# Kernel tuning notes

Measured on AMD Instinct MI355X. Metric: run time of the kernel, lower is better.

## Reference

```python
import jax, jax.numpy as jnp
import numpy as np

N = 8192          # number of nodes
F_IN = 256        # in_features
F_OUT = 128       # out_features


def setup_inputs() -> dict:
    key = jax.random.key(0)
    k1, k2, k3, k4 = jax.random.split(key, 4)
    input = jax.random.normal(k1, (N, F_IN), dtype=jnp.float32)
    adj = jax.random.uniform(k2, (N, N), dtype=jnp.float32)
    stdv = 1.0 / np.sqrt(F_OUT)
    weight = jax.random.uniform(k3, (F_IN, F_OUT), dtype=jnp.float32, minval=-stdv, maxval=stdv)
    bias = jax.random.uniform(k4, (F_OUT,), dtype=jnp.float32, minval=-stdv, maxval=stdv)
    return {"input": input, "adj": adj, "weight": weight, "bias": bias}


def reference(input, adj, weight, bias):
    # support = X @ W  [N, F_OUT]
    support = jnp.matmul(input, weight)
    # Subgraph block decomposition over a node partition is exactly A @ support:
    # block (k,i) computes adj[S_k][:, S_i] @ support[S_i] scatter-added into rows S_k.
    output = jnp.matmul(adj, support)  # [N, F_OUT]
    return output + bias
```

## Files before the change

### kernel.cpp

```cpp
#include <hip/hip_runtime.h>
#include <hip/hip_bf16.h>

#define N_NODES 8192
#define F_IN 256
#define F_OUT 128

#define SPLITK 4
#define KQ (N_NODES / SPLITK)
#define BK 64
#define NT (KQ / BK)
#define ABYTES 16384
#define BBYTES 16384
#define BUFB (ABYTES + BBYTES)

typedef __attribute__((ext_vector_type(4))) float f32x4;
typedef __attribute__((ext_vector_type(8))) short bf16x8;
typedef __attribute__((ext_vector_type(4))) unsigned int u32x4;

static __device__ __forceinline__ short bfr(float x) {
    __hip_bfloat16 h = __float2bfloat16(x);
    union { __hip_bfloat16 h; short s; } u; u.h = h;
    return u.s;
}

static __device__ __forceinline__ void gload16(const void* g, void* l) {
    __builtin_amdgcn_global_load_lds(
        (const __attribute__((address_space(1))) unsigned int*)g,
        (__attribute__((address_space(3))) unsigned int*)l, 16, 0, 0);
}

__global__ __launch_bounds__(256) void support_kernel(
        const float* __restrict__ X, const float* __restrict__ W,
        unsigned short* __restrict__ supT) {
    __shared__ float Xs[32][68];
    __shared__ float Ws[64][128];
    const int t = threadIdx.x;
    const int n0 = blockIdx.x * 32;
    const int tc = t & 31;
    const int tr = t >> 5;
    float acc[4][4];
    #pragma unroll
    for (int i = 0; i < 4; ++i)
        #pragma unroll
        for (int j = 0; j < 4; ++j) acc[i][j] = 0.f;

    for (int k0 = 0; k0 < F_IN; k0 += 64) {
        __syncthreads();
        {
            const int r = t >> 3, kc = (t & 7) * 8;
            const float* src = X + (size_t)(n0 + r) * F_IN + k0 + kc;
            f32x4 v0 = *(const f32x4*)src;
            f32x4 v1 = *(const f32x4*)(src + 4);
            *(f32x4*)&Xs[r][kc]     = v0;
            *(f32x4*)&Xs[r][kc + 4] = v1;
        }
        {
            const int col = t & 127, kb = t >> 7;
            #pragma unroll
            for (int i = 0; i < 32; ++i) {
                const int k = kb + i * 2;
                Ws[k][col] = W[(size_t)(k0 + k) * F_OUT + col];
            }
        }
        __syncthreads();
        #pragma unroll 8
        for (int k = 0; k < 64; ++k) {
            const f32x4 b = *(const f32x4*)&Ws[k][tc * 4];
            float a[4];
            #pragma unroll
            for (int i = 0; i < 4; ++i) a[i] = Xs[tr * 4 + i][k];
            #pragma unroll
            for (int i = 0; i < 4; ++i) {
                acc[i][0] += a[i] * b.x; acc[i][1] += a[i] * b.y;
                acc[i][2] += a[i] * b.z; acc[i][3] += a[i] * b.w;
            }
        }
    }
    #pragma unroll
    for (int j = 0; j < 4; ++j) {
        const int col = tc * 4 + j;
        #pragma unroll
        for (int i = 0; i < 4; ++i) {
            supT[(size_t)col * N_NODES + n0 + tr * 4 + i] =
                (unsigned short)bfr(acc[i][j]);
        }
    }
}

__global__ __launch_bounds__(512, 4) void gcn_kernel(
        const float* __restrict__ adj, const unsigned short* __restrict__ supT,
        const float* __restrict__ bias, float* __restrict__ out) {
    __shared__ char lds[2 * BUFB];
    const int t = threadIdx.x;
    const int l = t & 63;
    const int w = t >> 6;
    const int rb = blockIdx.x & 127;
    const int h = blockIdx.x >> 7;
    const int n0 = rb * 64;
    const int k0 = h * KQ;

    const int rA0 = 8 * w + (l >> 4);
    const int rA1 = rA0 + 4;
    const char* gA0 = (const char*)adj
        + ((size_t)(n0 + rA0) * N_NODES + k0) * 4 + (((l & 15) ^ (rA0 & 15)) * 16);
    const char* gA1 = (const char*)adj
        + ((size_t)(n0 + rA1) * N_NODES + k0) * 4 + (((l & 15) ^ (rA1 & 15)) * 16);
    const char* gB0 = (const char*)supT
        + ((size_t)(16 * w + (l >> 3)) * N_NODES + k0) * 2 + (((l & 7) ^ (l >> 3)) * 16);
    const char* gB1 = gB0 + (size_t)8 * N_NODES * 2;

    const int a_d0 = w * 2048;
    const int a_d1 = a_d0 + 1024;
    const int b_d0 = ABYTES + w * 2048;
    const int b_d1 = b_d0 + 1024;

    const int wm = w >> 2, wn = w & 3;
    const int aoff0 = (wm * 32 + (l & 15)) * 256;
    const int aoff1 = aoff0 + 16 * 256;
    const int akey = l & 15;
    const int ac0 = (l >> 4) * 2;
    const int boff0 = ABYTES + (wn * 32 + (l & 15)) * 128;
    const int boff1 = boff0 + 16 * 128;
    const int bkey = l & 7;
    const int cb0 = l >> 4;

    f32x4 acc00 = {0.f,0.f,0.f,0.f}, acc01 = {0.f,0.f,0.f,0.f};
    f32x4 acc10 = {0.f,0.f,0.f,0.f}, acc11 = {0.f,0.f,0.f,0.f};

#define PK(dst, a, b) \
    asm("v_cvt_pk_bf16_f32 %0, %1, %2" : "=v"(dst) : "v"(a), "v"(b))

#define STAGE(BUF) { \
    char* bb = &lds[(BUF) * BUFB]; \
    gload16(gA0, bb + a_d0); \
    gload16(gA1, bb + a_d1); \
    gload16(gB0, bb + b_d0); \
    gload16(gB1, bb + b_d1); \
    gA0 += 256; gA1 += 256; gB0 += 128; gB1 += 128; }

#define FENCE_BARRIER() { \
    asm volatile("s_waitcnt vmcnt(0)" ::: "memory"); \
    __builtin_amdgcn_sched_barrier(0); \
    __builtin_amdgcn_s_barrier(); \
    __builtin_amdgcn_sched_barrier(0); }

    STAGE(0);
    FENCE_BARRIER();

    for (int tt = 0; tt < NT; ++tt) {
        if (tt + 1 < NT) STAGE((tt + 1) & 1);

        const char* buf = &lds[(tt & 1) * BUFB];
        #pragma unroll
        for (int ks = 0; ks < 2; ++ks) {
            const int ca = ks * 8 + ac0;
            f32x4 a0lo = *(const f32x4*)(buf + aoff0 + (((ca    ) ^ akey) * 16));
            f32x4 a0hi = *(const f32x4*)(buf + aoff0 + (((ca + 1) ^ akey) * 16));
            f32x4 a1lo = *(const f32x4*)(buf + aoff1 + (((ca    ) ^ akey) * 16));
            f32x4 a1hi = *(const f32x4*)(buf + aoff1 + (((ca + 1) ^ akey) * 16));
            const int cb = ks * 4 + cb0;
            bf16x8 b0 = *(const bf16x8*)(buf + boff0 + ((cb ^ bkey) * 16));
            bf16x8 b1 = *(const bf16x8*)(buf + boff1 + ((cb ^ bkey) * 16));
            u32x4 p0, p1;
            PK(p0.x, a0lo.x, a0lo.y); PK(p0.y, a0lo.z, a0lo.w);
            PK(p0.z, a0hi.x, a0hi.y); PK(p0.w, a0hi.z, a0hi.w);
            PK(p1.x, a1lo.x, a1lo.y); PK(p1.y, a1lo.z, a1lo.w);
            PK(p1.z, a1hi.x, a1hi.y); PK(p1.w, a1hi.z, a1hi.w);
            bf16x8 am0 = __builtin_bit_cast(bf16x8, p0);
            bf16x8 am1 = __builtin_bit_cast(bf16x8, p1);
            acc00 = __builtin_amdgcn_mfma_f32_16x16x32_bf16(am0, b0, acc00, 0, 0, 0);
            acc01 = __builtin_amdgcn_mfma_f32_16x16x32_bf16(am0, b1, acc01, 0, 0, 0);
            acc10 = __builtin_amdgcn_mfma_f32_16x16x32_bf16(am1, b0, acc10, 0, 0, 0);
            acc11 = __builtin_amdgcn_mfma_f32_16x16x32_bf16(am1, b1, acc11, 0, 0, 0);
        }
        FENCE_BARRIER();
    }
#undef STAGE
#undef FENCE_BARRIER
#undef PK

    const int col = wn * 32 + (l & 15);
    const int row0 = n0 + wm * 32 + (l >> 4) * 4;
    const float bv0 = (h == 0) ? bias[col]      : 0.0f;
    const float bv1 = (h == 0) ? bias[col + 16] : 0.0f;
    #pragma unroll
    for (int i = 0; i < 4; ++i) {
        float* o0 = out + (size_t)(row0 + i) * F_OUT + col;
        float* o1 = out + (size_t)(row0 + i + 16) * F_OUT + col;
        unsafeAtomicAdd(&o0[0],  acc00[i] + bv0);
        unsafeAtomicAdd(&o0[16], acc01[i] + bv1);
        unsafeAtomicAdd(&o1[0],  acc10[i] + bv0);
        unsafeAtomicAdd(&o1[16], acc11[i] + bv1);
    }
}

extern "C" void kernel_launch(void* const* d_in, const int* in_sizes, int n_in,
                              void* d_out, int out_size, void* d_ws, size_t ws_size,
                              hipStream_t stream) {
    const float* input  = (const float*)d_in[0];
    const float* adj    = (const float*)d_in[1];
    const float* weight = (const float*)d_in[2];
    const float* bias   = (const float*)d_in[3];
    float* out = (float*)d_out;
    unsigned short* supT = (unsigned short*)d_ws;

    hipMemsetAsync(d_out, 0, (size_t)out_size * sizeof(float), stream);

    support_kernel<<<N_NODES / 32, 256, 0, stream>>>(input, weight, supT);
    gcn_kernel<<<128 * SPLITK, 512, 0, stream>>>(adj, supT, bias, out);
}
```

Measured before the change: 77.73 us.

## Halve row tile and triple-buffer adjacency loads with a two-stage prefetch

The gcn kernel now gives each block 32 rows instead of 64, which doubles the grid to 1024 blocks. The adjacency tile gets its own triple-buffered LDS region, prefetched two iterations ahead, while the support tile stays double-buffered. The wait before each barrier moves from vmcnt(0) to vmcnt(1), so the newest adjacency load can stay in flight across the barrier. This is meant to hide more HBM latency on the dominant adj stream and raise parallelism, but each block now does half the MFMA work per support tile and total L2 reads of the support matrix double.

```diff
diff --git a/kernel.cpp b/kernel.cpp
--- a/kernel.cpp
+++ b/kernel.cpp
@@ -9,13 +9,14 @@
 #define KQ (N_NODES / SPLITK)
 #define BK 64
 #define NT (KQ / BK)
-#define ABYTES 16384
+#define ABYTES 8192
 #define BBYTES 16384
-#define BUFB (ABYTES + BBYTES)
+#define AREG (3 * ABYTES)
+#define LDS_TOTAL (AREG + 2 * BBYTES)
 
 typedef __attribute__((ext_vector_type(4))) float f32x4;
 typedef __attribute__((ext_vector_type(8))) short bf16x8;
-typedef __attribute__((ext_vector_type(4))) unsigned int u32x4;
+typedef __attribute__((ext_vector_type(2))) unsigned int u32x2;
 
 static __device__ __forceinline__ short bfr(float x) {
     __hip_bfloat16 h = __float2bfloat16(x);
@@ -90,107 +91,109 @@
 __global__ __launch_bounds__(512, 4) void gcn_kernel(
         const float* __restrict__ adj, const unsigned short* __restrict__ supT,
         const float* __restrict__ bias, float* __restrict__ out) {
-    __shared__ char lds[2 * BUFB];
+    __shared__ char lds[LDS_TOTAL];
     const int t = threadIdx.x;
     const int l = t & 63;
     const int w = t >> 6;
-    const int rb = blockIdx.x & 127;
-    const int h = blockIdx.x >> 7;
-    const int n0 = rb * 64;
+    const int rb = blockIdx.x & 255;
+    const int h = blockIdx.x >> 8;
+    const int n0 = rb * 32;
     const int k0 = h * KQ;
 
-    const int rA0 = 8 * w + (l >> 4);
-    const int rA1 = rA0 + 4;
-    const char* gA0 = (const char*)adj
-        + ((size_t)(n0 + rA0) * N_NODES + k0) * 4 + (((l & 15) ^ (rA0 & 15)) * 16);
-    const char* gA1 = (const char*)adj
-        + ((size_t)(n0 + rA1) * N_NODES + k0) * 4 + (((l & 15) ^ (rA1 & 15)) * 16);
+    const int rA = 4 * w + (l >> 4);
+    const char* gA = (const char*)adj
+        + ((size_t)(n0 + rA) * N_NODES + k0) * 4 + (((l & 15) ^ (rA & 15)) * 16);
     const char* gB0 = (const char*)supT
         + ((size_t)(16 * w + (l >> 3)) * N_NODES + k0) * 2 + (((l & 7) ^ (l >> 3)) * 16);
     const char* gB1 = gB0 + (size_t)8 * N_NODES * 2;
 
-    const int a_d0 = w * 2048;
-    const int a_d1 = a_d0 + 1024;
-    const int b_d0 = ABYTES + w * 2048;
+    const int a_d  = w * 1024;
+    const int b_d0 = w * 2048;
     const int b_d1 = b_d0 + 1024;
 
     const int wm = w >> 2, wn = w & 3;
-    const int aoff0 = (wm * 32 + (l & 15)) * 256;
-    const int aoff1 = aoff0 + 16 * 256;
+    const int aoff = (wm * 16 + (l & 15)) * 256;
     const int akey = l & 15;
     const int ac0 = (l >> 4) * 2;
-    const int boff0 = ABYTES + (wn * 32 + (l & 15)) * 128;
+    const int boff0 = (wn * 32 + (l & 15)) * 128;
     const int boff1 = boff0 + 16 * 128;
     const int bkey = l & 7;
     const int cb0 = l >> 4;
 
-    f32x4 acc00 = {0.f,0.f,0.f,0.f}, acc01 = {0.f,0.f,0.f,0.f};
-    f32x4 acc10 = {0.f,0.f,0.f,0.f}, acc11 = {0.f,0.f,0.f,0.f};
+    f32x4 acc0 = {0.f,0.f,0.f,0.f}, acc1 = {0.f,0.f,0.f,0.f};
 
 #define PK(dst, a, b) \
     asm("v_cvt_pk_bf16_f32 %0, %1, %2" : "=v"(dst) : "v"(a), "v"(b))
 
-#define STAGE(BUF) { \
-    char* bb = &lds[(BUF) * BUFB]; \
-    gload16(gA0, bb + a_d0); \
-    gload16(gA1, bb + a_d1); \
+#define STAGE_B(BI) { \
+    char* bb = &lds[AREG + (BI) * BBYTES]; \
     gload16(gB0, bb + b_d0); \
     gload16(gB1, bb + b_d1); \
-    gA0 += 256; gA1 += 256; gB0 += 128; gB1 += 128; }
-
-#define FENCE_BARRIER() { \
-    asm volatile("s_waitcnt vmcnt(0)" ::: "memory"); \
-    __builtin_amdgcn_sched_barrier(0); \
-    __builtin_amdgcn_s_barrier(); \
-    __builtin_amdgcn_sched_barrier(0); }
-
-    STAGE(0);
-    FENCE_BARRIER();
-
+    gB0 += 128; gB1 += 128; }
+
+#define STAGE_A(AI) { \
+    gload16(gA, &lds[(AI) * ABYTES] + a_d); \
+    gA += 256; }
+
+    STAGE_B(0);
+    STAGE_A(0);
+    STAGE_A(1);
+    asm volatile("s_waitcnt vmcnt(1)" ::: "memory");
+    __builtin_amdgcn_sched_barrier(0);
+    __builtin_amdgcn_s_barrier();
+    __builtin_amdgcn_sched_barrier(0);
+
+    int ai = 0;
+    int bi = 0;
     for (int tt = 0; tt < NT; ++tt) {
-        if (tt + 1 < NT) STAGE((tt + 1) & 1);
-
-        const char* buf = &lds[(tt & 1) * BUFB];
+        if (tt + 1 < NT) STAGE_B(bi ^ 1);
+        if (tt + 2 < NT) { const int as = (ai >= 1) ? ai - 1 : 2; STAGE_A(as); }
+
+        const char* abuf = &lds[ai * ABYTES];
+        const char* bbuf = &lds[AREG + bi * BBYTES];
         #pragma unroll
         for (int ks = 0; ks < 2; ++ks) {
             const int ca = ks * 8 + ac0;
-            f32x4 a0lo = *(const f32x4*)(buf + aoff0 + (((ca    ) ^ akey) * 16));
-            f32x4 a0hi = *(const f32x4*)(buf + aoff0 + (((ca + 1) ^ akey) * 16));
-            f32x4 a1lo = *(const f32x4*)(buf + aoff1 + (((ca    ) ^ akey) * 16));
-            f32x4 a1hi = *(const f32x4*)(buf + aoff1 + (((ca + 1) ^ akey) * 16));
+            f32x4 alo = *(const f32x4*)(abuf + aoff + (((ca    ) ^ akey) * 16));
+            f32x4 ahi = *(const f32x4*)(abuf + aoff + (((ca + 1) ^ akey) * 16));
             const int cb = ks * 4 + cb0;
-            bf16x8 b0 = *(const bf16x8*)(buf + boff0 + ((cb ^ bkey) * 16));
-            bf16x8 b1 = *(const bf16x8*)(buf + boff1 + ((cb ^ bkey) * 16));
-            u32x4 p0, p1;
-            PK(p0.x, a0lo.x, a0lo.y); PK(p0.y, a0lo.z, a0lo.w);
-            PK(p0.z, a0hi.x, a0hi.y); PK(p0.w, a0hi.z, a0hi.w);
-            PK(p1.x, a1lo.x, a1lo.y); PK(p1.y, a1lo.z, a1lo.w);
-            PK(p1.z, a1hi.x, a1hi.y); PK(p1.w, a1hi.z, a1hi.w);
-            bf16x8 am0 = __builtin_bit_cast(bf16x8, p0);
-            bf16x8 am1 = __builtin_bit_cast(bf16x8, p1);
-            acc00 = __builtin_amdgcn_mfma_f32_16x16x32_bf16(am0, b0, acc00, 0, 0, 0);
-            acc01 = __builtin_amdgcn_mfma_f32_16x16x32_bf16(am0, b1, acc01, 0, 0, 0);
-            acc10 = __builtin_amdgcn_mfma_f32_16x16x32_bf16(am1, b0, acc10, 0, 0, 0);
-            acc11 = __builtin_amdgcn_mfma_f32_16x16x32_bf16(am1, b1, acc11, 0, 0, 0);
-        }
-        FENCE_BARRIER();
-    }
-#undef STAGE
-#undef FENCE_BARRIER
+            bf16x8 b0 = *(const bf16x8*)(bbuf + boff0 + ((cb ^ bkey) * 16));
+            bf16x8 b1 = *(const bf16x8*)(bbuf + boff1 + ((cb ^ bkey) * 16));
+            u32x2 plo, phi;
+            PK(plo.x, alo.x, alo.y); PK(plo.y, alo.z, alo.w);
+            PK(phi.x, ahi.x, ahi.y); PK(phi.y, ahi.z, ahi.w);
+            union { u32x2 u[2]; bf16x8 v; } am;
+            am.u[0] = plo; am.u[1] = phi;
+            acc0 = __builtin_amdgcn_mfma_f32_16x16x32_bf16(am.v, b0, acc0, 0, 0, 0);
+            acc1 = __builtin_amdgcn_mfma_f32_16x16x32_bf16(am.v, b1, acc1, 0, 0, 0);
+        }
+
+        if (tt < NT - 2) {
+            asm volatile("s_waitcnt vmcnt(1)" ::: "memory");
+        } else if (tt == NT - 2) {
+            asm volatile("s_waitcnt vmcnt(0)" ::: "memory");
+        }
+        if (tt < NT - 1) {
+            __builtin_amdgcn_sched_barrier(0);
+            __builtin_amdgcn_s_barrier();
+            __builtin_amdgcn_sched_barrier(0);
+        }
+        ai = (ai == 2) ? 0 : ai + 1;
+        bi ^= 1;
+    }
+#undef STAGE_A
+#undef STAGE_B
 #undef PK
 
     const int col = wn * 32 + (l & 15);
-    const int row0 = n0 + wm * 32 + (l >> 4) * 4;
+    const int row0 = n0 + wm * 16 + (l >> 4) * 4;
     const float bv0 = (h == 0) ? bias[col]      : 0.0f;
     const float bv1 = (h == 0) ? bias[col + 16] : 0.0f;
     #pragma unroll
     for (int i = 0; i < 4; ++i) {
-        float* o0 = out + (size_t)(row0 + i) * F_OUT + col;
-        float* o1 = out + (size_t)(row0 + i + 16) * F_OUT + col;
-        unsafeAtomicAdd(&o0[0],  acc00[i] + bv0);
-        unsafeAtomicAdd(&o0[16], acc01[i] + bv1);
-        unsafeAtomicAdd(&o1[0],  acc10[i] + bv0);
-        unsafeAtomicAdd(&o1[16], acc11[i] + bv1);
+        float* o = out + (size_t)(row0 + i) * F_OUT + col;
+        unsafeAtomicAdd(&o[0],  acc0[i] + bv0);
+        unsafeAtomicAdd(&o[16], acc1[i] + bv1);
     }
 }
 
@@ -205,7 +208,6 @@
     unsigned short* supT = (unsigned short*)d_ws;
 
     hipMemsetAsync(d_out, 0, (size_t)out_size * sizeof(float), stream);
-
     support_kernel<<<N_NODES / 32, 256, 0, stream>>>(input, weight, supT);
-    gcn_kernel<<<128 * SPLITK, 512, 0, stream>>>(adj, supT, bias, out);
-}
+    gcn_kernel<<<256 * SPLITK, 512, 0, stream>>>(adj, supT, bias, out);
+}
```

New measurement: 94.72 us. +21.9%, slower.

## Load support operand directly into registers and triple-buffer adj tiles in LDS

Applied to the files above, without the earlier changes.

The bf16 support operand is no longer staged through LDS. Each wave loads its B fragments straight from global memory into registers with inline global_load_dwordx4, double-buffered across even and odd register sets. The adj tile now uses a three-slot LDS ring with a partial vmcnt wait, so loads run two stages ahead. This cuts LDS traffic and footprint and deepens prefetch, at the cost of more VGPRs and redundant global reads of supT across waves. The partial-wait counts depend on how the hand-written asm loads are ordered.

```diff
diff --git a/kernel.cpp b/kernel.cpp
--- a/kernel.cpp
+++ b/kernel.cpp
@@ -10,8 +10,6 @@
 #define BK 64
 #define NT (KQ / BK)
 #define ABYTES 16384
-#define BBYTES 16384
-#define BUFB (ABYTES + BBYTES)
 
 typedef __attribute__((ext_vector_type(4))) float f32x4;
 typedef __attribute__((ext_vector_type(8))) short bf16x8;
@@ -90,7 +88,7 @@
 __global__ __launch_bounds__(512, 4) void gcn_kernel(
         const float* __restrict__ adj, const unsigned short* __restrict__ supT,
         const float* __restrict__ bias, float* __restrict__ out) {
-    __shared__ char lds[2 * BUFB];
+    __shared__ char lds[3 * ABYTES];
     const int t = threadIdx.x;
     const int l = t & 63;
     const int w = t >> 6;
@@ -105,78 +103,102 @@
         + ((size_t)(n0 + rA0) * N_NODES + k0) * 4 + (((l & 15) ^ (rA0 & 15)) * 16);
     const char* gA1 = (const char*)adj
         + ((size_t)(n0 + rA1) * N_NODES + k0) * 4 + (((l & 15) ^ (rA1 & 15)) * 16);
-    const char* gB0 = (const char*)supT
-        + ((size_t)(16 * w + (l >> 3)) * N_NODES + k0) * 2 + (((l & 7) ^ (l >> 3)) * 16);
-    const char* gB1 = gB0 + (size_t)8 * N_NODES * 2;
-
     const int a_d0 = w * 2048;
     const int a_d1 = a_d0 + 1024;
-    const int b_d0 = ABYTES + w * 2048;
-    const int b_d1 = b_d0 + 1024;
 
     const int wm = w >> 2, wn = w & 3;
+    const int f0 = wn * 32 + (l & 15);
+    unsigned int boff0 = (unsigned)f0 * (N_NODES * 2) + (unsigned)(k0 * 2)
+                       + ((l >> 4) * 16);
+    unsigned int boff1 = boff0 + 16u * (N_NODES * 2);
+
     const int aoff0 = (wm * 32 + (l & 15)) * 256;
     const int aoff1 = aoff0 + 16 * 256;
     const int akey = l & 15;
     const int ac0 = (l >> 4) * 2;
-    const int boff0 = ABYTES + (wn * 32 + (l & 15)) * 128;
-    const int boff1 = boff0 + 16 * 128;
-    const int bkey = l & 7;
-    const int cb0 = l >> 4;
 
     f32x4 acc00 = {0.f,0.f,0.f,0.f}, acc01 = {0.f,0.f,0.f,0.f};
     f32x4 acc10 = {0.f,0.f,0.f,0.f}, acc11 = {0.f,0.f,0.f,0.f};
 
+    u32x4 bE0, bE1, bE2, bE3;
+    u32x4 bO0, bO1, bO2, bO3;
+
 #define PK(dst, a, b) \
     asm("v_cvt_pk_bf16_f32 %0, %1, %2" : "=v"(dst) : "v"(a), "v"(b))
 
-#define STAGE(BUF) { \
-    char* bb = &lds[(BUF) * BUFB]; \
+#define BLD(dst, off, imm) \
+    asm volatile("global_load_dwordx4 %0, %1, %2 offset:" imm \
+                 : "=v"(dst) : "v"(off), "s"(supT) : "memory")
+
+#define STAGE_BREG(SET) { \
+    BLD(b##SET##0, boff0, "0");  BLD(b##SET##1, boff0, "64"); \
+    BLD(b##SET##2, boff1, "0");  BLD(b##SET##3, boff1, "64"); \
+    boff0 += 128; boff1 += 128; }
+
+#define STAGE_A(AI) { \
+    char* bb = &lds[(AI) * ABYTES]; \
     gload16(gA0, bb + a_d0); \
     gload16(gA1, bb + a_d1); \
-    gload16(gB0, bb + b_d0); \
-    gload16(gB1, bb + b_d1); \
-    gA0 += 256; gA1 += 256; gB0 += 128; gB1 += 128; }
-
-#define FENCE_BARRIER() { \
-    asm volatile("s_waitcnt vmcnt(0)" ::: "memory"); \
+    gA0 += 256; gA1 += 256; }
+
+#define FENCE(IMM) { \
+    asm volatile("s_waitcnt vmcnt(" IMM ")" ::: "memory"); \
     __builtin_amdgcn_sched_barrier(0); \
     __builtin_amdgcn_s_barrier(); \
     __builtin_amdgcn_sched_barrier(0); }
 
-    STAGE(0);
-    FENCE_BARRIER();
-
-    for (int tt = 0; tt < NT; ++tt) {
-        if (tt + 1 < NT) STAGE((tt + 1) & 1);
-
-        const char* buf = &lds[(tt & 1) * BUFB];
-        #pragma unroll
-        for (int ks = 0; ks < 2; ++ks) {
-            const int ca = ks * 8 + ac0;
-            f32x4 a0lo = *(const f32x4*)(buf + aoff0 + (((ca    ) ^ akey) * 16));
-            f32x4 a0hi = *(const f32x4*)(buf + aoff0 + (((ca + 1) ^ akey) * 16));
-            f32x4 a1lo = *(const f32x4*)(buf + aoff1 + (((ca    ) ^ akey) * 16));
-            f32x4 a1hi = *(const f32x4*)(buf + aoff1 + (((ca + 1) ^ akey) * 16));
-            const int cb = ks * 4 + cb0;
-            bf16x8 b0 = *(const bf16x8*)(buf + boff0 + ((cb ^ bkey) * 16));
-            bf16x8 b1 = *(const bf16x8*)(buf + boff1 + ((cb ^ bkey) * 16));
-            u32x4 p0, p1;
-            PK(p0.x, a0lo.x, a0lo.y); PK(p0.y, a0lo.z, a0lo.w);
-            PK(p0.z, a0hi.x, a0hi.y); PK(p0.w, a0hi.z, a0hi.w);
-            PK(p1.x, a1lo.x, a1lo.y); PK(p1.y, a1lo.z, a1lo.w);
-            PK(p1.z, a1hi.x, a1hi.y); PK(p1.w, a1hi.z, a1hi.w);
-            bf16x8 am0 = __builtin_bit_cast(bf16x8, p0);
-            bf16x8 am1 = __builtin_bit_cast(bf16x8, p1);
-            acc00 = __builtin_amdgcn_mfma_f32_16x16x32_bf16(am0, b0, acc00, 0, 0, 0);
-            acc01 = __builtin_amdgcn_mfma_f32_16x16x32_bf16(am0, b1, acc01, 0, 0, 0);
-            acc10 = __builtin_amdgcn_mfma_f32_16x16x32_bf16(am1, b0, acc10, 0, 0, 0);
-            acc11 = __builtin_amdgcn_mfma_f32_16x16x32_bf16(am1, b1, acc11, 0, 0, 0);
-        }
-        FENCE_BARRIER();
-    }
-#undef STAGE
-#undef FENCE_BARRIER
+#define HALF(ABUF, CA, BF0, BF1) { \
+    f32x4 a0lo = *(const f32x4*)((ABUF) + aoff0 + ((((CA)    ) ^ akey) * 16)); \
+    f32x4 a0hi = *(const f32x4*)((ABUF) + aoff0 + ((((CA) + 1) ^ akey) * 16)); \
+    f32x4 a1lo = *(const f32x4*)((ABUF) + aoff1 + ((((CA)    ) ^ akey) * 16)); \
+    f32x4 a1hi = *(const f32x4*)((ABUF) + aoff1 + ((((CA) + 1) ^ akey) * 16)); \
+    u32x4 p0, p1; \
+    PK(p0.x, a0lo.x, a0lo.y); PK(p0.y, a0lo.z, a0lo.w); \
+    PK(p0.z, a0hi.x, a0hi.y); PK(p0.w, a0hi.z, a0hi.w); \
+    PK(p1.x, a1lo.x, a1lo.y); PK(p1.y, a1lo.z, a1lo.w); \
+    PK(p1.z, a1hi.x, a1hi.y); PK(p1.w, a1hi.z, a1hi.w); \
+    bf16x8 am0 = __builtin_bit_cast(bf16x8, p0); \
+    bf16x8 am1 = __builtin_bit_cast(bf16x8, p1); \
+    acc00 = __builtin_amdgcn_mfma_f32_16x16x32_bf16(am0, __builtin_bit_cast(bf16x8, BF0), acc00, 0, 0, 0); \
+    acc01 = __builtin_amdgcn_mfma_f32_16x16x32_bf16(am0, __builtin_bit_cast(bf16x8, BF1), acc01, 0, 0, 0); \
+    acc10 = __builtin_amdgcn_mfma_f32_16x16x32_bf16(am1, __builtin_bit_cast(bf16x8, BF0), acc10, 0, 0, 0); \
+    acc11 = __builtin_amdgcn_mfma_f32_16x16x32_bf16(am1, __builtin_bit_cast(bf16x8, BF1), acc11, 0, 0, 0); }
+
+#define COMPUTE(AI, SET) { \
+    const char* abuf = &lds[(AI) * ABYTES]; \
+    HALF(abuf, ac0,     b##SET##0, b##SET##2); \
+    HALF(abuf, ac0 + 8, b##SET##1, b##SET##3); }
+
+    STAGE_BREG(E);
+    STAGE_A(0);
+    STAGE_A(1);
+    FENCE("2");
+
+    int ai = 0;
+    for (int t2 = 0; t2 < NT - 2; t2 += 2) {
+        STAGE_BREG(O);
+        { const int an = (ai >= 1) ? ai - 1 : 2; STAGE_A(an); }
+        COMPUTE(ai, E);
+        FENCE("2");
+        ai = (ai == 2) ? 0 : ai + 1;
+        STAGE_BREG(E);
+        { const int an = (ai >= 1) ? ai - 1 : 2; STAGE_A(an); }
+        COMPUTE(ai, O);
+        FENCE("2");
+        ai = (ai == 2) ? 0 : ai + 1;
+    }
+    STAGE_BREG(O);
+    COMPUTE(ai, E);
+    FENCE("0");
+    ai = (ai == 2) ? 0 : ai + 1;
+    COMPUTE(ai, O);
+
+#undef COMPUTE
+#undef HALF
+#undef FENCE
+#undef STAGE_A
+#undef STAGE_BREG
+#undef BLD
 #undef PK
 
     const int col = wn * 32 + (l & 15);
@@ -205,7 +227,6 @@
     unsigned short* supT = (unsigned short*)d_ws;
 
     hipMemsetAsync(d_out, 0, (size_t)out_size * sizeof(float), stream);
-
     support_kernel<<<N_NODES / 32, 256, 0, stream>>>(input, weight, supT);
     gcn_kernel<<<128 * SPLITK, 512, 0, stream>>>(adj, supT, bias, out);
 }
```

Result: slower. 109.4 us (+40.7%).

## Load adj tiles into registers, convert to bf16 once, store bf16 in LDS

Applied to the files above, without the earlier changes.

The adj tiles are now fetched with global_load_dwordx4 into registers two tiles ahead and packed to bf16 once per element. The packed values are written to a smaller bf16 LDS buffer, while supT still streams directly to LDS. This removes the redundant fp32 LDS traffic and the repeated conversion in the MFMA loop, and cuts LDS per block so more blocks can be resident. The price is more registers and hand-tuned vmcnt waits, which depend on an exact count of outstanding loads and break if that count is wrong.

```diff
diff --git a/kernel.cpp b/kernel.cpp
--- a/kernel.cpp
+++ b/kernel.cpp
@@ -9,9 +9,10 @@
 #define KQ (N_NODES / SPLITK)
 #define BK 64
 #define NT (KQ / BK)
-#define ABYTES 16384
-#define BBYTES 16384
-#define BUFB (ABYTES + BBYTES)
+#define A_LDS 8192
+#define B_LDS 16384
+#define B_BASE (2 * A_LDS)
+#define LDS_TOTAL (2 * A_LDS + 2 * B_LDS)
 
 typedef __attribute__((ext_vector_type(4))) float f32x4;
 typedef __attribute__((ext_vector_type(8))) short bf16x8;
@@ -90,7 +91,7 @@
 __global__ __launch_bounds__(512, 4) void gcn_kernel(
         const float* __restrict__ adj, const unsigned short* __restrict__ supT,
         const float* __restrict__ bias, float* __restrict__ out) {
-    __shared__ char lds[2 * BUFB];
+    __shared__ char lds[LDS_TOTAL];
     const int t = threadIdx.x;
     const int l = t & 63;
     const int w = t >> 6;
@@ -99,85 +100,124 @@
     const int n0 = rb * 64;
     const int k0 = h * KQ;
 
-    const int rA0 = 8 * w + (l >> 4);
-    const int rA1 = rA0 + 4;
-    const char* gA0 = (const char*)adj
-        + ((size_t)(n0 + rA0) * N_NODES + k0) * 4 + (((l & 15) ^ (rA0 & 15)) * 16);
-    const char* gA1 = (const char*)adj
-        + ((size_t)(n0 + rA1) * N_NODES + k0) * 4 + (((l & 15) ^ (rA1 & 15)) * 16);
+    const int arow = 8 * w + (l >> 3);
+    unsigned int aoffv = (unsigned)(((size_t)(n0 + arow) * N_NODES + k0
+                                     + (l & 7) * 8) * 4);
+    const int awoff = arow * 128 + (((l & 7) ^ ((l >> 3) & 7)) * 16);
+
     const char* gB0 = (const char*)supT
         + ((size_t)(16 * w + (l >> 3)) * N_NODES + k0) * 2 + (((l & 7) ^ (l >> 3)) * 16);
     const char* gB1 = gB0 + (size_t)8 * N_NODES * 2;
-
-    const int a_d0 = w * 2048;
-    const int a_d1 = a_d0 + 1024;
-    const int b_d0 = ABYTES + w * 2048;
+    const int b_d0 = w * 2048;
     const int b_d1 = b_d0 + 1024;
 
     const int wm = w >> 2, wn = w & 3;
-    const int aoff0 = (wm * 32 + (l & 15)) * 256;
-    const int aoff1 = aoff0 + 16 * 256;
-    const int akey = l & 15;
-    const int ac0 = (l >> 4) * 2;
-    const int boff0 = ABYTES + (wn * 32 + (l & 15)) * 128;
+    const int aoff0 = (wm * 32 + (l & 15)) * 128;
+    const int aoff1 = aoff0 + 16 * 128;
+    const int akey = l & 7;
+    const int boff0 = (wn * 32 + (l & 15)) * 128;
     const int boff1 = boff0 + 16 * 128;
     const int bkey = l & 7;
-    const int cb0 = l >> 4;
+    const int cg = l >> 4;
 
     f32x4 acc00 = {0.f,0.f,0.f,0.f}, acc01 = {0.f,0.f,0.f,0.f};
     f32x4 acc10 = {0.f,0.f,0.f,0.f}, acc11 = {0.f,0.f,0.f,0.f};
 
+    f32x4 aE0, aE1, aO0, aO1;
+
 #define PK(dst, a, b) \
     asm("v_cvt_pk_bf16_f32 %0, %1, %2" : "=v"(dst) : "v"(a), "v"(b))
 
-#define STAGE(BUF) { \
-    char* bb = &lds[(BUF) * BUFB]; \
-    gload16(gA0, bb + a_d0); \
-    gload16(gA1, bb + a_d1); \
+#define BLDA(dst, imm) \
+    asm volatile("global_load_dwordx4 %0, %1, %2 offset:" imm \
+                 : "=v"(dst) : "v"(aoffv), "s"(adj) : "memory")
+
+#define STAGE_AREG(r0, r1) { \
+    BLDA(r0, "0"); \
+    BLDA(r1, "16"); \
+    aoffv += 256; }
+
+#define STAGE_B(P) { \
+    char* bb = &lds[B_BASE + (P) * B_LDS]; \
     gload16(gB0, bb + b_d0); \
     gload16(gB1, bb + b_d1); \
-    gA0 += 256; gA1 += 256; gB0 += 128; gB1 += 128; }
-
-#define FENCE_BARRIER() { \
-    asm volatile("s_waitcnt vmcnt(0)" ::: "memory"); \
-    __builtin_amdgcn_sched_barrier(0); \
+    gB0 += 128; gB1 += 128; }
+
+#define CVT_WRITE(WP, r0, r1) { \
+    u32x4 q; \
+    PK(q.x, r0.x, r0.y); PK(q.y, r0.z, r0.w); \
+    PK(q.z, r1.x, r1.y); PK(q.w, r1.z, r1.w); \
+    *(u32x4*)(&lds[(WP) * A_LDS] + awoff) = q; }
+
+#define COMPUTE(P) { \
+    const char* ab = &lds[(P) * A_LDS]; \
+    const char* bb = &lds[B_BASE + (P) * B_LDS]; \
+    _Pragma("unroll") \
+    for (int ks = 0; ks < 2; ++ks) { \
+        const int c = ks * 4 + cg; \
+        bf16x8 a0 = *(const bf16x8*)(ab + aoff0 + ((c ^ akey) * 16)); \
+        bf16x8 a1 = *(const bf16x8*)(ab + aoff1 + ((c ^ akey) * 16)); \
+        bf16x8 b0 = *(const bf16x8*)(bb + boff0 + ((c ^ bkey) * 16)); \
+        bf16x8 b1 = *(const bf16x8*)(bb + boff1 + ((c ^ bkey) * 16)); \
+        acc00 = __builtin_amdgcn_mfma_f32_16x16x32_bf16(a0, b0, acc00, 0, 0, 0); \
+        acc01 = __builtin_amdgcn_mfma_f32_16x16x32_bf16(a0, b1, acc01, 0, 0, 0); \
+        acc10 = __builtin_amdgcn_mfma_f32_16x16x32_bf16(a1, b0, acc10, 0, 0, 0); \
+        acc11 = __builtin_amdgcn_mfma_f32_16x16x32_bf16(a1, b1, acc11, 0, 0, 0); \
+    } }
+
+#define WAIT(IMM) { \
+    asm volatile("s_waitcnt vmcnt(" IMM ")" ::: "memory"); \
+    __builtin_amdgcn_sched_barrier(0); }
+
+#define WAITL(IMM) { \
+    asm volatile("s_waitcnt vmcnt(" IMM ") lgkmcnt(0)" ::: "memory"); \
+    __builtin_amdgcn_sched_barrier(0); }
+
+#define BAR() { \
     __builtin_amdgcn_s_barrier(); \
     __builtin_amdgcn_sched_barrier(0); }
 
-    STAGE(0);
-    FENCE_BARRIER();
-
-    for (int tt = 0; tt < NT; ++tt) {
-        if (tt + 1 < NT) STAGE((tt + 1) & 1);
-
-        const char* buf = &lds[(tt & 1) * BUFB];
-        #pragma unroll
-        for (int ks = 0; ks < 2; ++ks) {
-            const int ca = ks * 8 + ac0;
-            f32x4 a0lo = *(const f32x4*)(buf + aoff0 + (((ca    ) ^ akey) * 16));
-            f32x4 a0hi = *(const f32x4*)(buf + aoff0 + (((ca + 1) ^ akey) * 16));
-            f32x4 a1lo = *(const f32x4*)(buf + aoff1 + (((ca    ) ^ akey) * 16));
-            f32x4 a1hi = *(const f32x4*)(buf + aoff1 + (((ca + 1) ^ akey) * 16));
-            const int cb = ks * 4 + cb0;
-            bf16x8 b0 = *(const bf16x8*)(buf + boff0 + ((cb ^ bkey) * 16));
-            bf16x8 b1 = *(const bf16x8*)(buf + boff1 + ((cb ^ bkey) * 16));
-            u32x4 p0, p1;
-            PK(p0.x, a0lo.x, a0lo.y); PK(p0.y, a0lo.z, a0lo.w);
-            PK(p0.z, a0hi.x, a0hi.y); PK(p0.w, a0hi.z, a0hi.w);
-            PK(p1.x, a1lo.x, a1lo.y); PK(p1.y, a1lo.z, a1lo.w);
-            PK(p1.z, a1hi.x, a1hi.y); PK(p1.w, a1hi.z, a1hi.w);
-            bf16x8 am0 = __builtin_bit_cast(bf16x8, p0);
-            bf16x8 am1 = __builtin_bit_cast(bf16x8, p1);
-            acc00 = __builtin_amdgcn_mfma_f32_16x16x32_bf16(am0, b0, acc00, 0, 0, 0);
-            acc01 = __builtin_amdgcn_mfma_f32_16x16x32_bf16(am0, b1, acc01, 0, 0, 0);
-            acc10 = __builtin_amdgcn_mfma_f32_16x16x32_bf16(am1, b0, acc10, 0, 0, 0);
-            acc11 = __builtin_amdgcn_mfma_f32_16x16x32_bf16(am1, b1, acc11, 0, 0, 0);
-        }
-        FENCE_BARRIER();
-    }
-#undef STAGE
-#undef FENCE_BARRIER
+    STAGE_AREG(aE0, aE1);
+    STAGE_B(0);
+    STAGE_AREG(aO0, aO1);
+    WAIT("4");
+    CVT_WRITE(0, aE0, aE1);
+    WAITL("2");
+    BAR();
+
+    for (int t2 = 0; t2 + 3 < NT; t2 += 2) {
+        STAGE_B(1);
+        STAGE_AREG(aE0, aE1);
+        COMPUTE(0);
+        WAIT("4");
+        CVT_WRITE(1, aO0, aO1);
+        WAITL("2");
+        BAR();
+        STAGE_B(0);
+        STAGE_AREG(aO0, aO1);
+        COMPUTE(1);
+        WAIT("4");
+        CVT_WRITE(0, aE0, aE1);
+        WAITL("2");
+        BAR();
+    }
+    STAGE_B(1);
+    COMPUTE(0);
+    WAIT("2");
+    CVT_WRITE(1, aO0, aO1);
+    WAITL("0");
+    BAR();
+    COMPUTE(1);
+
 #undef PK
+#undef BLDA
+#undef STAGE_AREG
+#undef STAGE_B
+#undef CVT_WRITE
+#undef COMPUTE
+#undef WAIT
+#undef WAITL
+#undef BAR
 
     const int col = wn * 32 + (l & 15);
     const int row0 = n0 + wm * 32 + (l >> 4) * 4;
@@ -205,7 +245,6 @@
     unsigned short* supT = (unsigned short*)d_ws;
 
     hipMemsetAsync(d_out, 0, (size_t)out_size * sizeof(float), stream);
-
     support_kernel<<<N_NODES / 32, 256, 0, stream>>>(input, weight, supT);
     gcn_kernel<<<128 * SPLITK, 512, 0, stream>>>(adj, supT, bias, out);
 }
```

After: 79.87 us. 2.8% more time.
